# Kernel optimization log

Hardware: AMD Instinct MI355X
Metric: run time of the kernel (lower is better)

The kernel has to match this reference:

```python
import jax, jax.numpy as jnp
import numpy as np

K = 3  # kernel_size
P = K // 2


def setup_inputs() -> dict:
    key = jax.random.key(0)
    k1, k2 = jax.random.split(key)
    x = jax.random.normal(k1, (8, 64, 256, 256), dtype=jnp.float32)
    alpha = jnp.full((1, 64, 1, 1), 0.1, dtype=jnp.float32)
    return {"x": x, "alpha": alpha}


def reference(x, alpha):
    # Equivalent to F.unfold(x, K, padding=P) -> abs-diff from center -> sum over K*K -> residual.
    b, c, h, w = x.shape
    xp = jnp.pad(x, ((0, 0), (0, 0), (P, P), (P, P)))  # zero padding, same as F.unfold
    diff_sum = jnp.zeros_like(x)
    for di in range(K):
        for dj in range(K):
            neighbor = xp[:, :, di:di + h, dj:dj + w]
            diff_sum = diff_sum + jnp.abs(x - neighbor)
    return x + alpha * diff_sum
```

## Files before the change

kernel.cpp:

```cpp
#include <hip/hip_runtime.h>
#include <stdint.h>


typedef float f32x4 __attribute__((ext_vector_type(4)));

constexpr int H = 256;
constexpr int W = 256;
constexpr int C = 64;
constexpr int SLAB = 16;
constexpr int NR   = SLAB + 2;
constexpr int RSTR = 264;

typedef const uint32_t __attribute__((address_space(1)))* gas_t;
typedef uint32_t __attribute__((address_space(3)))* las_t;

__global__ __launch_bounds__(256) void adc_kernel(
    const float* __restrict__ x,
    const float* __restrict__ alpha,
    float* __restrict__ out)
{
    __shared__ float lds[NR * RSTR];

    const int tid  = threadIdx.x;
    const int lane = tid & 63;
    const int wave = tid >> 6;

    const int n     = blockIdx.x;
    const int xcd   = n & 7;
    const int local = n >> 3;
    const int img   = ((local >> 4) << 3) + xcd;
    const int slab  = local & 15;
    const int y0    = slab * SLAB;

    const float a = alpha[img & (C - 1)];
    const float* imgp = x   + (long)img * (H * W);
    float*       outp = out + (long)img * (H * W);

    if (tid < NR) {
        *(f32x4*)&lds[tid * RSTR] = (f32x4){0.f, 0.f, 0.f, 0.f};
        lds[tid * RSTR + 260] = 0.f;
    }

#pragma unroll
    for (int r = wave; r < NR; r += 4) {
        const int g = y0 + r - 1;
        if (g >= 0 && g < H) {
            const float* gsrc = imgp + (long)g * W + lane * 4;
            __builtin_amdgcn_global_load_lds((gas_t)gsrc,
                                             (las_t)&lds[r * RSTR + 4],
                                             16, 0, 0);
        } else {
            *(f32x4*)&lds[r * RSTR + 4 + lane * 4] =
                (f32x4){0.f, 0.f, 0.f, 0.f};
        }
    }
    __syncthreads();

    const int r0    = wave * 4 + 1;
    const int cbase = 4 + lane * 4;

    f32x4 eq[3];
    float eL[3], eR[3];
#pragma unroll
    for (int k = 0; k < 2; ++k) {
        const int rr = r0 - 1 + k;
        eq[k] = *(const f32x4*)&lds[rr * RSTR + cbase];
        eL[k] = lds[rr * RSTR + cbase - 1];
        eR[k] = lds[rr * RSTR + cbase + 4];
    }

    float* orow0 = outp + (long)(y0 + wave * 4) * W + lane * 4;

#pragma unroll
    for (int o = 0; o < 4; ++o) {
        const int s = (o + 2) % 3, t = o % 3, m = (o + 1) % 3;
        const int rr = r0 + o + 1;
        eq[s] = *(const f32x4*)&lds[rr * RSTR + cbase];
        eL[s] = lds[rr * RSTR + cbase - 1];
        eR[s] = lds[rr * RSTR + cbase + 4];

        float e[3][6];
#pragma unroll
        for (int k = 0; k < 3; ++k) {
            const int kk = (k == 0) ? t : ((k == 1) ? m : s);
            e[k][0] = eL[kk];
            e[k][1] = eq[kk].x; e[k][2] = eq[kk].y;
            e[k][3] = eq[kk].z; e[k][4] = eq[kk].w;
            e[k][5] = eR[kk];
        }

        f32x4 res;
#pragma unroll
        for (int j = 0; j < 4; ++j) {
            const float xc = e[1][j + 1];
            float sacc = 0.f;
#pragma unroll
            for (int r2 = 0; r2 < 3; ++r2)
#pragma unroll
                for (int d = 0; d < 3; ++d)
                    sacc += fabsf(xc - e[r2][j + d]);
            res[j] = fmaf(a, sacc, xc);
        }
        __builtin_nontemporal_store(res, (f32x4*)(orow0 + o * W));
    }
}

extern "C" void kernel_launch(void* const* d_in, const int* in_sizes, int n_in,
                              void* d_out, int out_size, void* d_ws, size_t ws_size,
                              hipStream_t stream)
{
    const float* x     = (const float*)d_in[0];
    const float* alpha = (const float*)d_in[1];
    float*       out   = (float*)d_out;

    const int grid = 8 * C * (H / SLAB);
    adc_kernel<<<grid, 256, 0, stream>>>(x, alpha, out);
}
```

Before: 228.1 us.

## Double-buffer LDS slabs and process four slabs per block with prefetch

Each block now handles four consecutive 16-row slabs instead of one. It uses two LDS buffers so the async global-to-LDS load of the next slab is issued before the current slab is computed. The aim is to hide global load latency behind the stencil arithmetic and to spend less time on per-block setup and halo zeroing. In exchange the grid is four times smaller, LDS use per block doubles, and each slab still ends with a barrier that may drain outstanding stores.

```diff
diff --git a/kernel.cpp b/kernel.cpp
--- a/kernel.cpp
+++ b/kernel.cpp
@@ -7,55 +7,38 @@
 constexpr int H = 256;
 constexpr int W = 256;
 constexpr int C = 64;
-constexpr int SLAB = 16;
-constexpr int NR   = SLAB + 2;
-constexpr int RSTR = 264;
+constexpr int SLAB  = 16;
+constexpr int NR    = SLAB + 2;
+constexpr int RSTR  = 264;
+constexpr int NSLAB = 4;
 
 typedef const uint32_t __attribute__((address_space(1)))* gas_t;
 typedef uint32_t __attribute__((address_space(3)))* las_t;
 
-__global__ __launch_bounds__(256) void adc_kernel(
-    const float* __restrict__ x,
-    const float* __restrict__ alpha,
-    float* __restrict__ out)
+__device__ __forceinline__ void stage_slab(const float* __restrict__ imgp,
+                                           int y0, float* __restrict__ buf,
+                                           int wave, int lane)
 {
-    __shared__ float lds[NR * RSTR];
-
-    const int tid  = threadIdx.x;
-    const int lane = tid & 63;
-    const int wave = tid >> 6;
-
-    const int n     = blockIdx.x;
-    const int xcd   = n & 7;
-    const int local = n >> 3;
-    const int img   = ((local >> 4) << 3) + xcd;
-    const int slab  = local & 15;
-    const int y0    = slab * SLAB;
-
-    const float a = alpha[img & (C - 1)];
-    const float* imgp = x   + (long)img * (H * W);
-    float*       outp = out + (long)img * (H * W);
-
-    if (tid < NR) {
-        *(f32x4*)&lds[tid * RSTR] = (f32x4){0.f, 0.f, 0.f, 0.f};
-        lds[tid * RSTR + 260] = 0.f;
-    }
-
 #pragma unroll
     for (int r = wave; r < NR; r += 4) {
         const int g = y0 + r - 1;
         if (g >= 0 && g < H) {
             const float* gsrc = imgp + (long)g * W + lane * 4;
             __builtin_amdgcn_global_load_lds((gas_t)gsrc,
-                                             (las_t)&lds[r * RSTR + 4],
+                                             (las_t)&buf[r * RSTR + 4],
                                              16, 0, 0);
         } else {
-            *(f32x4*)&lds[r * RSTR + 4 + lane * 4] =
+            *(f32x4*)&buf[r * RSTR + 4 + lane * 4] =
                 (f32x4){0.f, 0.f, 0.f, 0.f};
         }
     }
-    __syncthreads();
+}
 
+__device__ __forceinline__ void compute_slab(const float* __restrict__ buf,
+                                             float* __restrict__ outp,
+                                             int y0, float a,
+                                             int wave, int lane)
+{
     const int r0    = wave * 4 + 1;
     const int cbase = 4 + lane * 4;
 
@@ -64,9 +47,9 @@
 #pragma unroll
     for (int k = 0; k < 2; ++k) {
         const int rr = r0 - 1 + k;
-        eq[k] = *(const f32x4*)&lds[rr * RSTR + cbase];
-        eL[k] = lds[rr * RSTR + cbase - 1];
-        eR[k] = lds[rr * RSTR + cbase + 4];
+        eq[k] = *(const f32x4*)&buf[rr * RSTR + cbase];
+        eL[k] = buf[rr * RSTR + cbase - 1];
+        eR[k] = buf[rr * RSTR + cbase + 4];
     }
 
     float* orow0 = outp + (long)(y0 + wave * 4) * W + lane * 4;
@@ -75,9 +58,9 @@
     for (int o = 0; o < 4; ++o) {
         const int s = (o + 2) % 3, t = o % 3, m = (o + 1) % 3;
         const int rr = r0 + o + 1;
-        eq[s] = *(const f32x4*)&lds[rr * RSTR + cbase];
-        eL[s] = lds[rr * RSTR + cbase - 1];
-        eR[s] = lds[rr * RSTR + cbase + 4];
+        eq[s] = *(const f32x4*)&buf[rr * RSTR + cbase];
+        eL[s] = buf[rr * RSTR + cbase - 1];
+        eR[s] = buf[rr * RSTR + cbase + 4];
 
         float e[3][6];
 #pragma unroll
@@ -105,6 +88,46 @@
     }
 }
 
+__global__ __launch_bounds__(256) void adc_kernel(
+    const float* __restrict__ x,
+    const float* __restrict__ alpha,
+    float* __restrict__ out)
+{
+    __shared__ float lds[2][NR * RSTR];
+
+    const int tid  = threadIdx.x;
+    const int lane = tid & 63;
+    const int wave = tid >> 6;
+
+    const int n     = blockIdx.x;
+    const int xcd   = n & 7;
+    const int local = n >> 3;
+    const int img   = ((local >> 2) << 3) + xcd;
+    const int ybase = (local & 3) * (NSLAB * SLAB);
+
+    const float a = alpha[img & (C - 1)];
+    const float* imgp = x   + (long)img * (H * W);
+    float*       outp = out + (long)img * (H * W);
+
+    if (tid < 2 * NR) {
+        float* row = &lds[tid >= NR][(tid % NR) * RSTR];
+        *(f32x4*)row = (f32x4){0.f, 0.f, 0.f, 0.f};
+        row[260] = 0.f;
+    }
+
+    stage_slab(imgp, ybase, &lds[0][0], wave, lane);
+    __syncthreads();
+
+#pragma unroll
+    for (int k = 0; k < NSLAB; ++k) {
+        if (k + 1 < NSLAB)
+            stage_slab(imgp, ybase + (k + 1) * SLAB,
+                       &lds[(k + 1) & 1][0], wave, lane);
+        compute_slab(&lds[k & 1][0], outp, ybase + k * SLAB, a, wave, lane);
+        __syncthreads();
+    }
+}
+
 extern "C" void kernel_launch(void* const* d_in, const int* in_sizes, int n_in,
                               void* d_out, int out_size, void* d_ws, size_t ws_size,
                               hipStream_t stream)
@@ -113,6 +136,6 @@
     const float* alpha = (const float*)d_in[1];
     float*       out   = (float*)d_out;
 
-    const int grid = 8 * C * (H / SLAB);
+    const int grid = 8 * C * (H / (NSLAB * SLAB));
     adc_kernel<<<grid, 256, 0, stream>>>(x, alpha, out);
 }
```

Result: slower. 235.3 us (+3.1%).
